# Performance work log

Measured on AMD Instinct MI355X. Metric: run time of the kernel, lower is better.

## Reference

```python
import jax, jax.numpy as jnp
import numpy as np

N, E, B, C, L, HLS = 30000, 480000, 64, 128, 3, 64
PARAM_NAMES = ['Wq','bq','Wk','bk','Wv','bv','Wskip','bskip','lstm_Wih_f','lstm_Whh_f','lstm_bih_f','lstm_bhh_f','lstm_Wih_b','lstm_Whh_b','lstm_bih_b','lstm_bhh_b','att_W','att_b','gP_W1','gP_b1','gP_W2','gP_b2','gT_W1','gT_b1','gT_W2','gT_b2','m_W0','m_b0','m_W1','m_b1','m_W2','m_b2']


def setup_inputs() -> dict:
    key = jax.random.key(0)
    ks = iter(jax.random.split(key, 64))
    rn = lambda shape: jax.random.normal(next(ks), shape, dtype=jnp.float32) * 0.05
    inp = {
        'x': jax.random.normal(next(ks), (N, C), dtype=jnp.float32),
        'edge_index': jax.random.randint(next(ks), (2, E), 0, N, dtype=jnp.int32),
        'batch': jnp.sort(jax.random.randint(next(ks), (N,), 0, B, dtype=jnp.int32)),
        'hls_attr': jax.random.normal(next(ks), (B, HLS), dtype=jnp.float32),
        'Wq': rn((L, C, C)), 'bq': rn((L, C)),
        'Wk': rn((L, C, C)), 'bk': rn((L, C)),
        'Wv': rn((L, C, C)), 'bv': rn((L, C)),
        'Wskip': rn((L, C, C)), 'bskip': rn((L, C)),
        'lstm_Wih_f': rn((4 * C, C)), 'lstm_Whh_f': rn((4 * C, C)),
        'lstm_bih_f': rn((4 * C,)), 'lstm_bhh_f': rn((4 * C,)),
        'lstm_Wih_b': rn((4 * C, C)), 'lstm_Whh_b': rn((4 * C, C)),
        'lstm_bih_b': rn((4 * C,)), 'lstm_bhh_b': rn((4 * C,)),
        'att_W': rn((2 * C, 1)), 'att_b': rn((1,)),
        'gP_W1': rn((C, C)), 'gP_b1': rn((C,)), 'gP_W2': rn((C, 1)), 'gP_b2': rn((1,)),
        'gT_W1': rn((C, C)), 'gT_b1': rn((C,)), 'gT_W2': rn((C, 1)), 'gT_b2': rn((1,)),
        'm_W0': rn((2 * C + HLS, 64)), 'm_b0': rn((64,)),
        'm_W1': rn((64, 64)), 'm_b1': rn((64,)),
        'm_W2': rn((64, 1)), 'm_b2': rn((1,)),
    }
    return inp


def _segment_softmax(logits, seg, num):
    m = jax.ops.segment_max(logits, seg, num_segments=num)
    e = jnp.exp(logits - m[seg])
    d = jax.ops.segment_sum(e, seg, num_segments=num)
    return e / d[seg]


def _lstm(xs, Wih, Whh, bih, bhh):
    # xs: [L, N, C] -> outputs [L, N, H]
    H = Whh.shape[1]
    h0 = jnp.zeros((xs.shape[1], H), xs.dtype)
    bias = bih + bhh
    def step(carry, xt):
        h, c = carry
        z = xt @ Wih.T + h @ Whh.T + bias
        i, f, g, o = jnp.split(z, 4, axis=-1)
        c = jax.nn.sigmoid(f) * c + jax.nn.sigmoid(i) * jnp.tanh(g)
        h = jax.nn.sigmoid(o) * jnp.tanh(c)
        return (h, c), h
    _, hs = jax.lax.scan(step, (h0, h0), xs)
    return hs


def _gate_pool(x, batch, W1, b1, W2, b2):
    gate = jax.nn.relu(x @ W1 + b1) @ W2 + b2          # [N, 1]
    gate = _segment_softmax(gate[:, 0], batch, B)[:, None]
    return jax.ops.segment_sum(gate * x, batch, num_segments=B)


def _forward(x, edge_index, batch, hls_attr, Wq, bq, Wk, bk, Wv, bv, Wskip, bskip,
             lstm_Wih_f, lstm_Whh_f, lstm_bih_f, lstm_bhh_f,
             lstm_Wih_b, lstm_Whh_b, lstm_bih_b, lstm_bhh_b,
             att_W, att_b, gP_W1, gP_b1, gP_W2, gP_b2, gT_W1, gT_b1, gT_W2, gT_b2,
             m_W0, m_b0, m_W1, m_b1, m_W2, m_b2):
    src, dst = edge_index[0], edge_index[1]
    scale = 1.0 / jnp.sqrt(jnp.asarray(C, jnp.float32))
    h_list = []
    for i in range(L):
        q = x @ Wq[i] + bq[i]
        k = x @ Wk[i] + bk[i]
        v = x @ Wv[i] + bv[i]
        logits = jnp.sum(q[dst] * k[src], axis=-1) * scale   # [E]
        alpha = _segment_softmax(logits, dst, N)             # per-dst softmax
        agg = jax.ops.segment_sum(alpha[:, None] * v[src], dst, num_segments=N)
        x = jax.nn.relu(agg + x @ Wskip[i] + bskip[i])       # TransformerConv + root skip, then ReLU
        h_list.append(x)
    xs = jnp.stack(h_list)                                   # [L, N, C]
    hf = _lstm(xs, lstm_Wih_f, lstm_Whh_f, lstm_bih_f, lstm_bhh_f)
    hb = _lstm(xs[::-1], lstm_Wih_b, lstm_Whh_b, lstm_bih_b, lstm_bhh_b)[::-1]
    hcat = jnp.concatenate([hf, hb], axis=-1)                # [L, N, 2C]
    a = jax.nn.softmax((hcat @ att_W)[..., 0] + att_b[0], axis=0)  # softmax over layers
    x = jnp.sum(a[..., None] * xs, axis=0)                   # [N, C] JK-LSTM output
    out_P = _gate_pool(x, batch, gP_W1, gP_b1, gP_W2, gP_b2)
    out_T = _gate_pool(x, batch, gT_W1, gT_b1, gT_W2, gT_b2)
    h = jnp.concatenate([out_P, out_T, hls_attr], axis=-1)   # [B, 2C+HLS]
    h = jax.nn.relu(h @ m_W0 + m_b0)
    h = jax.nn.relu(h @ m_W1 + m_b1)
    return h @ m_W2 + m_b2                                   # [B, 1]


def reference(x, edge_index, batch, hls_attr, Wq, bq, Wk, bk, Wv, bv, Wskip, bskip,
              lstm_Wih_f, lstm_Whh_f, lstm_bih_f, lstm_bhh_f,
              lstm_Wih_b, lstm_Whh_b, lstm_bih_b, lstm_bhh_b,
              att_W, att_b, gP_W1, gP_b1, gP_W2, gP_b2, gT_W1, gT_b1, gT_W2, gT_b2,
              m_W0, m_b0, m_W1, m_b1, m_W2, m_b2):
    return _forward(x, edge_index, batch, hls_attr, Wq, bq, Wk, bk, Wv, bv, Wskip, bskip,
                    lstm_Wih_f, lstm_Whh_f, lstm_bih_f, lstm_bhh_f,
                    lstm_Wih_b, lstm_Whh_b, lstm_bih_b, lstm_bhh_b,
                    att_W, att_b, gP_W1, gP_b1, gP_W2, gP_b2, gT_W1, gT_b1, gT_W2, gT_b2,
                    m_W0, m_b0, m_W1, m_b1, m_W2, m_b2)
```

## Files before the change

kernel.cpp:

```cpp
#include <hip/hip_runtime.h>
#include <math.h>

#define NN 30000
#define EE 480000
#define BB 64
#define CC 128
#define LLAYERS 3
#define HLSD 64
#define GXPAD 472

typedef __attribute__((ext_vector_type(8))) short bf16x8;
typedef __attribute__((ext_vector_type(4))) float f32x4;
typedef unsigned short u16;

__device__ inline unsigned short f2bf(float f){
  unsigned u = __float_as_uint(f);
  u += 0x7fffu + ((u >> 16) & 1u);
  return (unsigned short)(u >> 16);
}
__device__ inline float bf2f(unsigned short h){
  return __uint_as_float(((unsigned)h) << 16);
}
__device__ inline float fsig(float z){
  return __builtin_amdgcn_rcpf(1.f + __expf(-z));
}
__device__ inline float ftanh(float z){
  return 1.f - 2.f*__builtin_amdgcn_rcpf(1.f + __expf(2.f*z));
}

__global__ void k_hist(const int* __restrict__ dst, int* __restrict__ counts, int E){
  int e = blockIdx.x*256 + threadIdx.x;
  if (e < E) atomicAdd(&counts[dst[e]], 1);
}
__global__ void k_scan_block(const int* __restrict__ counts, int* __restrict__ row_ptr,
                             int* __restrict__ bsums, int n){
  __shared__ int sm[256];
  int i = blockIdx.x*256 + threadIdx.x;
  int v = (i < n) ? counts[i] : 0;
  sm[threadIdx.x] = v; __syncthreads();
  for (int off = 1; off < 256; off <<= 1){
    int t = (threadIdx.x >= off) ? sm[threadIdx.x - off] : 0;
    __syncthreads();
    sm[threadIdx.x] += t;
    __syncthreads();
  }
  if (i < n) row_ptr[i+1] = sm[threadIdx.x];
  if (threadIdx.x == 255) bsums[blockIdx.x] = sm[255];
}
__global__ void k_scan_bsums(const int* __restrict__ bsums, int* __restrict__ bexcl, int nb){
  int tid = threadIdx.x;
  int lane = tid & 63, wid = tid >> 6;
  int v = (tid < nb) ? bsums[tid] : 0;
  int s = v;
  #pragma unroll
  for (int o = 1; o < 64; o <<= 1){
    int t = __shfl_up(s, o, 64);
    if (lane >= o) s += t;
  }
  __shared__ int wsum[2];
  if (lane == 63) wsum[wid] = s;
  __syncthreads();
  int add = (wid == 1) ? wsum[0] : 0;
  if (tid < nb) bexcl[tid] = s - v + add;
}
__global__ void k_scan_add(int* __restrict__ row_ptr, const int* __restrict__ bexcl, int n){
  int i = blockIdx.x*256 + threadIdx.x;
  if (i < n) row_ptr[i+1] += bexcl[i >> 8];
  if (i == 0) row_ptr[0] = 0;
}
__global__ void k_fill(const int* __restrict__ src, const int* __restrict__ dst,
                       const int* __restrict__ row_ptr, int* __restrict__ fill,
                       int* __restrict__ esrc, int E){
  int e = blockIdx.x*256 + threadIdx.x;
  if (e < E){
    int d = dst[e];
    int pos = row_ptr[d] + atomicAdd(&fill[d], 1);
    esrc[pos] = src[e];
  }
}

struct PrepPtrs {
  const float* tsrc[14]; unsigned short* tdst[14];
  const float* csrc[4];  unsigned short* cdst[4];
  const float *bihf, *bhhf, *bihb, *bhhb;
  float *cbf, *cbb;
};
__global__ __launch_bounds__(256) void k_prep(PrepPtrs p){
  int b = blockIdx.x, tid = threadIdx.x;
  if (b < 14){
    const float* s = p.tsrc[b]; unsigned short* d = p.tdst[b];
    for (int i = tid; i < 16384; i += 256){
      int k = i >> 7, n = i & 127;
      d[n*128 + k] = f2bf(s[i]);
    }
  } else if (b < 30){
    int m = (b - 14) >> 2, ch = (b - 14) & 3;
    const float* s = p.csrc[m] + ch*16384; unsigned short* d = p.cdst[m] + ch*16384;
    for (int i = tid; i < 16384; i += 256) d[i] = f2bf(s[i]);
  } else {
    for (int i = tid; i < 512; i += 256){
      p.cbf[i] = p.bihf[i] + p.bhhf[i];
      p.cbb[i] = p.bihb[i] + p.bhhb[i];
    }
  }
}
__global__ __launch_bounds__(256) void k_cvt_x(const float* __restrict__ src,
                                               unsigned short* __restrict__ dst, int n8){
  int i = blockIdx.x*256 + threadIdx.x;
  if (i >= n8) return;
  float4 a = *(const float4*)(src + (size_t)i*8);
  float4 b = *(const float4*)(src + (size_t)i*8 + 4);
  union { unsigned short u[8]; uint4 v; } o;
  o.u[0]=f2bf(a.x); o.u[1]=f2bf(a.y); o.u[2]=f2bf(a.z); o.u[3]=f2bf(a.w);
  o.u[4]=f2bf(b.x); o.u[5]=f2bf(b.y); o.u[6]=f2bf(b.z); o.u[7]=f2bf(b.w);
  *(uint4*)(dst + (size_t)i*8) = o.v;
}

struct Quad { const unsigned short* Bt[4]; const float* bias[4]; };

template<int RELU, int OUTBF16>
__global__ __launch_bounds__(256) void k_mfma_gemm(
    const unsigned short* __restrict__ A0, Quad qd,
    float* __restrict__ Cf, unsigned short* __restrict__ Cb,
    int M, int ldC, int colsPerMat)
{
  __shared__ unsigned short As0[64*128];
  __shared__ unsigned short Bs0[64*128];

  const int tid = threadIdx.x;
  const int row0 = blockIdx.x*64;
  const int colg0 = blockIdx.y*64;
  const int mi = colg0 / colsPerMat;
  const int nloc = colg0 - mi*colsPerMat;
  const unsigned short* Bt0 = qd.Bt[mi];

  #pragma unroll
  for (int i = 0; i < 4; i++){
    int ch = tid + i*256;
    int r = ch >> 4, c16 = ch & 15;
    int gr = row0 + r;
    uint4 av = make_uint4(0,0,0,0);
    if (gr < M) av = *(const uint4*)(A0 + (size_t)gr*128 + c16*8);
    *(uint4*)((char*)As0 + ((r*256 + c16*16) ^ ((r&7)<<4))) = av;
    uint4 bv = *(const uint4*)(Bt0 + (size_t)(nloc + r)*128 + c16*8);
    *(uint4*)((char*)Bs0 + ((r*256 + c16*16) ^ ((r&7)<<4))) = bv;
  }
  __syncthreads();

  const int w = tid >> 6, l = tid & 63;
  const int lr = l & 15, lhi = l >> 4;

  f32x4 acc[4];
  #pragma unroll
  for (int f = 0; f < 4; f++){ acc[f][0]=0.f; acc[f][1]=0.f; acc[f][2]=0.f; acc[f][3]=0.f; }

  #pragma unroll
  for (int kt = 0; kt < 4; kt++){
    int arow = w*16 + lr;
    bf16x8 a = *(const bf16x8*)((const char*)As0 + ((arow*256 + kt*64 + lhi*16) ^ ((arow&7)<<4)));
    #pragma unroll
    for (int f = 0; f < 4; f++){
      int brow = f*16 + lr;
      bf16x8 b = *(const bf16x8*)((const char*)Bs0 + ((brow*256 + kt*64 + lhi*16) ^ ((brow&7)<<4)));
      acc[f] = __builtin_amdgcn_mfma_f32_16x16x32_bf16(a, b, acc[f], 0, 0, 0);
    }
  }

  const float* bias = qd.bias[mi];
  #pragma unroll
  for (int f = 0; f < 4; f++){
    int colg = colg0 + f*16 + lr;
    float bv = bias ? bias[nloc + f*16 + lr] : 0.f;
    #pragma unroll
    for (int r = 0; r < 4; r++){
      int grow = row0 + w*16 + lhi*4 + r;
      if (grow < M){
        float v = acc[f][r] + bv;
        if (RELU) v = fmaxf(v, 0.f);
        if (OUTBF16) Cb[(size_t)grow*ldC + colg] = f2bf(v);
        else         Cf[(size_t)grow*ldC + colg] = v;
      }
    }
  }
}

struct LstmArgs {
  const u16 *Xf, *Xb, *Hf, *Hb;
  const u16 *Wihf, *Whhf, *Wihb, *Whhb;
  const float *cbf, *cbb;
  u16 *Hof, *Hob;
  u16 *Cf, *Cb2;
  float *scF, *scB;
  const float* attW;
  int M;
};
template<int FIRST>
__global__ __launch_bounds__(256) void k_lstm2(LstmArgs a){
  __shared__ unsigned short As[64*128];
  __shared__ unsigned short Bs[128*128];
  const int bid = blockIdx.x;
  const int rowtile = bid % GXPAD;
  const int yy = bid / GXPAD;
  const int M = a.M;
  if (rowtile*64 >= M) return;
  const int dir = yy >> 2;
  const int t0 = (yy & 3)*32;
  const u16* X = dir ? a.Xb : a.Xf;
  const u16* H = dir ? a.Hb : a.Hf;
  const u16* Wih = dir ? a.Wihb : a.Wihf;
  const u16* Whh = dir ? a.Whhb : a.Whhf;
  const float* cbias = dir ? a.cbb : a.cbf;
  u16* Hout = dir ? a.Hob : a.Hof;
  u16* Cst = dir ? a.Cb2 : a.Cf;
  float* score = dir ? a.scB : a.scF;
  const float* attW = a.attW + dir*128;

  const int tid = threadIdx.x;
  const int row0 = rowtile*64;
  const int w = tid >> 6, l = tid & 63, lr = l & 15, lhi = l >> 4;

  f32x4 acc[8];
  #pragma unroll
  for (int f = 0; f < 8; f++){ acc[f][0]=0.f; acc[f][1]=0.f; acc[f][2]=0.f; acc[f][3]=0.f; }

  const int npair = FIRST ? 1 : 2;
  for (int pair = 0; pair < npair; pair++){
    const unsigned short* A  = pair ? H   : X;
    const unsigned short* Bt = pair ? Whh : Wih;
    if (pair) __syncthreads();
    #pragma unroll
    for (int i = 0; i < 4; i++){
      int ch = tid + i*256;
      int r = ch >> 4, c16 = ch & 15;
      int gr = row0 + r;
      uint4 av = make_uint4(0,0,0,0);
      if (gr < M) av = *(const uint4*)(A + (size_t)gr*128 + c16*8);
      *(uint4*)((char*)As + ((r*256 + c16*16) ^ ((r&7)<<4))) = av;
    }
    #pragma unroll
    for (int i = 0; i < 8; i++){
      int ch = tid + i*256;
      int r = ch >> 4, c16 = ch & 15;
      int gr = (r >> 5)*128 + t0 + (r & 31);
      uint4 bv = *(const uint4*)(Bt + (size_t)gr*128 + c16*8);
      *(uint4*)((char*)Bs + ((r*256 + c16*16) ^ ((r&7)<<4))) = bv;
    }
    __syncthreads();
    #pragma unroll
    for (int kt = 0; kt < 4; kt++){
      int arow = w*16 + lr;
      bf16x8 av = *(const bf16x8*)((const char*)As + ((arow*256 + kt*64 + lhi*16) ^ ((arow&7)<<4)));
      #pragma unroll
      for (int f = 0; f < 8; f++){
        int brow = f*16 + lr;
        bf16x8 bv = *(const bf16x8*)((const char*)Bs + ((brow*256 + kt*64 + lhi*16) ^ ((brow&7)<<4)));
        acc[f] = __builtin_amdgcn_mfma_f32_16x16x32_bf16(av, bv, acc[f], 0, 0, 0);
      }
    }
  }

  float sc[4] = {0.f, 0.f, 0.f, 0.f};
  #pragma unroll
  for (int cb = 0; cb < 2; cb++){
    int t = t0 + cb*16 + lr;
    float aw  = attW[t];
    float bi  = cbias[t];
    float bf_ = cbias[128 + t];
    float bg  = cbias[256 + t];
    float bo  = cbias[384 + t];
    #pragma unroll
    for (int r = 0; r < 4; r++){
      int grow = row0 + w*16 + lhi*4 + r;
      if (grow < M){
        float zi = acc[0+cb][r] + bi;
        float zf = acc[2+cb][r] + bf_;
        float zg = acc[4+cb][r] + bg;
        float zo = acc[6+cb][r] + bo;
        float cp = FIRST ? 0.f : bf2f(Cst[(size_t)grow*128 + t]);
        float cn = fsig(zf)*cp + fsig(zi)*ftanh(zg);
        float hn = fsig(zo)*ftanh(cn);
        Cst[(size_t)grow*128 + t] = f2bf(cn);
        Hout[(size_t)grow*128 + t] = f2bf(hn);
        sc[r] += hn * aw;
      }
    }
  }
  #pragma unroll
  for (int r = 0; r < 4; r++){
    float p = sc[r];
    p += __shfl_xor(p, 1, 64);
    p += __shfl_xor(p, 2, 64);
    p += __shfl_xor(p, 4, 64);
    p += __shfl_xor(p, 8, 64);
    if (lr == 0){
      int grow = row0 + w*16 + lhi*4 + r;
      if (grow < M) atomicAdd(&score[grow], p);
    }
  }
}

__global__ __launch_bounds__(256) void k_attn(
    const unsigned short* __restrict__ qkvs, const int* __restrict__ row_ptr,
    const int* __restrict__ esrc, unsigned short* __restrict__ xout, int n)
{
  int wid = threadIdx.x >> 6, lane = threadIdx.x & 63;
  int dst = blockIdx.x*4 + wid;
  if (dst >= n) return;
  const int g = lane >> 4, j = lane & 15;
  const size_t drow = (size_t)dst*512;

  bf16x8 qv = *(const bf16x8*)(qkvs + drow + j*8);
  float qf[8];
  #pragma unroll
  for (int i = 0; i < 8; i++) qf[i] = bf2f((unsigned short)qv[i]);

  const int rs = row_ptr[dst], re = row_ptr[dst+1];
  const float scale2 = 0.08838834764831845f * 1.4426950408889634f;
  float den = 0.f;
  float acc[8];
  #pragma unroll
  for (int i = 0; i < 8; i++) acc[i] = 0.f;

  int e = rs + g;
  if (e < re){
    int s = esrc[e];
    const unsigned short* sr = qkvs + (size_t)s*512 + j*8;
    bf16x8 kc = *(const bf16x8*)(sr + 128);
    bf16x8 vc = *(const bf16x8*)(sr + 256);
    while (true){
      int en = e + 4;
      bool havenext = en < re;
      bf16x8 kn, vn;
      if (havenext){
        int sn = esrc[en];
        const unsigned short* srn = qkvs + (size_t)sn*512 + j*8;
        kn = *(const bf16x8*)(srn + 128);
        vn = *(const bf16x8*)(srn + 256);
      }
      float d = qf[0]*bf2f((unsigned short)kc[0]);
      #pragma unroll
      for (int i = 1; i < 8; i++) d += qf[i]*bf2f((unsigned short)kc[i]);
      d += __shfl_xor(d, 1, 64);
      d += __shfl_xor(d, 2, 64);
      d += __shfl_xor(d, 4, 64);
      d += __shfl_xor(d, 8, 64);
      float wgt = exp2f(d * scale2);
      den += wgt;
      #pragma unroll
      for (int i = 0; i < 8; i++)
        acc[i] += wgt*bf2f((unsigned short)vc[i]);
      if (!havenext) break;
      e = en; kc = kn; vc = vn;
    }
  }

  #pragma unroll
  for (int o = 16; o <= 32; o <<= 1){
    den += __shfl_xor(den, o, 64);
    #pragma unroll
    for (int i = 0; i < 8; i++)
      acc[i] += __shfl_xor(acc[i], o, 64);
  }

  if (g == 0){
    bf16x8 sk = *(const bf16x8*)(qkvs + drow + 384 + j*8);
    float inv = (re > rs) ? 1.f/den : 0.f;
    union { unsigned short u[8]; uint4 v; } o8;
    #pragma unroll
    for (int i = 0; i < 8; i++){
      float v = acc[i]*inv + bf2f((unsigned short)sk[i]);
      o8.u[i] = f2bf(fmaxf(v, 0.f));
    }
    *(uint4*)(xout + (size_t)dst*128 + j*8) = o8.v;
  }
}

__global__ void k_jk_weights(const float* __restrict__ sF, const float* __restrict__ sB,
                             const float* __restrict__ attb, float* __restrict__ a, int n){
  int i = blockIdx.x*256 + threadIdx.x;
  if (i >= n) return;
  float s0 = sF[i]       + sB[i]       + attb[0];
  float s1 = sF[n+i]     + sB[n+i]     + attb[0];
  float s2 = sF[2*n+i]   + sB[2*n+i]   + attb[0];
  float mm = fmaxf(s0, fmaxf(s1, s2));
  float e0 = __expf(s0-mm), e1 = __expf(s1-mm), e2 = __expf(s2-mm);
  float d = e0 + e1 + e2;
  a[i] = e0/d; a[n+i] = e1/d; a[2*n+i] = e2/d;
}
__global__ void k_jk_combine(const float* __restrict__ a,
                             const unsigned short* __restrict__ x0,
                             const unsigned short* __restrict__ x1,
                             const unsigned short* __restrict__ x2,
                             float* __restrict__ xjk, unsigned short* __restrict__ xjkb, int n){
  int i8 = blockIdx.x*256 + threadIdx.x;
  if (i8 >= n*16) return;
  int node = i8 >> 4;
  float a0 = a[node], a1 = a[n+node], a2 = a[2*n+node];
  bf16x8 v0 = *(const bf16x8*)(x0 + (size_t)i8*8);
  bf16x8 v1 = *(const bf16x8*)(x1 + (size_t)i8*8);
  bf16x8 v2 = *(const bf16x8*)(x2 + (size_t)i8*8);
  float r[8];
  union { unsigned short u[8]; uint4 v; } ob;
  #pragma unroll
  for (int i = 0; i < 8; i++){
    r[i] = a0*bf2f((unsigned short)v0[i]) + a1*bf2f((unsigned short)v1[i]) + a2*bf2f((unsigned short)v2[i]);
    ob.u[i] = f2bf(r[i]);
  }
  float4* xo = (float4*)(xjk + (size_t)i8*8);
  xo[0] = make_float4(r[0], r[1], r[2], r[3]);
  xo[1] = make_float4(r[4], r[5], r[6], r[7]);
  *(uint4*)(xjkb + (size_t)i8*8) = ob.v;
}

__global__ __launch_bounds__(256) void k_rowdot2(
    const unsigned short* __restrict__ g,
    const float* __restrict__ w2P, const float* __restrict__ w2T,
    const float* __restrict__ b2P, const float* __restrict__ b2T,
    float* __restrict__ glP, float* __restrict__ glT, int n)
{
  int wid = threadIdx.x >> 6, lane = threadIdx.x & 63;
  int node = blockIdx.x*4 + wid;
  if (node >= n) return;
  ushort4 gv = *(const ushort4*)(g + (size_t)node*256 + lane*4);
  const float* w = (lane >= 32) ? w2T : w2P;
  int c0 = (lane*4) & 127;
  float4 wv = *(const float4*)(w + c0);
  float p = bf2f(gv.x)*wv.x + bf2f(gv.y)*wv.y + bf2f(gv.z)*wv.z + bf2f(gv.w)*wv.w;
  #pragma unroll
  for (int o = 1; o < 32; o <<= 1) p += __shfl_xor(p, o, 64);
  if (lane == 0)  glP[node] = p + b2P[0];
  if (lane == 32) glT[node] = p + b2T[0];
}

__global__ void k_segbounds(const int* __restrict__ batch, int* __restrict__ segp, int n){
  int i = blockIdx.x*256 + threadIdx.x;
  if (i >= n) return;
  int b = batch[i];
  int bp = (i == 0) ? -1 : batch[i-1];
  for (int s = bp+1; s <= b; s++) segp[s] = i;
  if (i == n-1){
    for (int s = b+1; s <= BB; s++) segp[s] = n;
  }
}

__global__ __launch_bounds__(256) void k_seg_stats(
    const float* __restrict__ glP, const float* __restrict__ glT,
    const int* __restrict__ segp, float4* __restrict__ stats)
{
  const int b = blockIdx.x, tid = threadIdx.x;
  const int s0 = segp[b], s1 = segp[b+1];
  __shared__ float sred[8];

  float mP = -INFINITY, mT = -INFINITY;
  for (int i = s0 + tid; i < s1; i += 256){
    mP = fmaxf(mP, glP[i]);
    mT = fmaxf(mT, glT[i]);
  }
  #pragma unroll
  for (int o = 1; o < 64; o <<= 1){
    mP = fmaxf(mP, __shfl_xor(mP, o, 64));
    mT = fmaxf(mT, __shfl_xor(mT, o, 64));
  }
  if ((tid & 63) == 0){ sred[(tid >> 6)*2] = mP; sred[(tid >> 6)*2 + 1] = mT; }
  __syncthreads();
  mP = fmaxf(fmaxf(sred[0], sred[2]), fmaxf(sred[4], sred[6]));
  mT = fmaxf(fmaxf(sred[1], sred[3]), fmaxf(sred[5], sred[7]));
  __syncthreads();

  float dP = 0.f, dT = 0.f;
  for (int i = s0 + tid; i < s1; i += 256){
    dP += __expf(glP[i] - mP);
    dT += __expf(glT[i] - mT);
  }
  #pragma unroll
  for (int o = 1; o < 64; o <<= 1){
    dP += __shfl_xor(dP, o, 64);
    dT += __shfl_xor(dT, o, 64);
  }
  if ((tid & 63) == 0){ sred[(tid >> 6)*2] = dP; sred[(tid >> 6)*2 + 1] = dT; }
  __syncthreads();
  if (tid == 0){
    dP = sred[0] + sred[2] + sred[4] + sred[6];
    dT = sred[1] + sred[3] + sred[5] + sred[7];
    float4 st;
    st.x = mP; st.y = mT;
    st.z = (dP > 0.f) ? 1.f/dP : 0.f;
    st.w = (dT > 0.f) ? 1.f/dT : 0.f;
    stats[b] = st;
  }
}

__global__ __launch_bounds__(256) void k_poolsum(
    const float* __restrict__ xjk, const int* __restrict__ segp,
    const float* __restrict__ glP, const float* __restrict__ glT,
    const float4* __restrict__ stats,
    float* __restrict__ poolP, float* __restrict__ poolT)
{
  const int b = blockIdx.x;
  const int s0 = segp[b], s1 = segp[b+1];
  const float4 st = stats[b];
  const int half = threadIdx.x >> 7, c = threadIdx.x & 127;
  const int stream = blockIdx.y*2 + half;
  float aP = 0.f, aT = 0.f;
  for (int i = s0 + stream; i < s1; i += 32){
    float eP = __expf(glP[i] - st.x);
    float eT = __expf(glT[i] - st.y);
    float xv = xjk[(size_t)i*128 + c];
    aP += eP*xv; aT += eT*xv;
  }
  if (aP != 0.f) atomicAdd(&poolP[(size_t)b*128 + c], aP*st.z);
  if (aT != 0.f) atomicAdd(&poolT[(size_t)b*128 + c], aT*st.w);
}

__global__ __launch_bounds__(64) void k_mlp(
    const float* __restrict__ poolP, const float* __restrict__ poolT, const float* __restrict__ hls,
    const float* __restrict__ W0, const float* __restrict__ b0,
    const float* __restrict__ W1, const float* __restrict__ b1,
    const float* __restrict__ W2, const float* __restrict__ b2, float* __restrict__ out)
{
  __shared__ float hin[320];
  __shared__ float h1[64];
  int b = blockIdx.x, j = threadIdx.x;
  for (int i = j; i < 320; i += 64){
    float vv;
    if (i < 128)      vv = poolP[(size_t)b*128 + i];
    else if (i < 256) vv = poolT[(size_t)b*128 + (i-128)];
    else              vv = hls[(size_t)b*64 + (i-256)];
    hin[i] = vv;
  }
  __syncthreads();
  float s = b0[j];
  for (int kk = 0; kk < 320; kk++) s += hin[kk] * W0[kk*64 + j];
  h1[j] = fmaxf(s, 0.f);
  __syncthreads();
  float s2 = b1[j];
  for (int kk = 0; kk < 64; kk++) s2 += h1[kk] * W1[kk*64 + j];
  float h2 = fmaxf(s2, 0.f);
  float p = h2 * W2[j];
  #pragma unroll
  for (int o = 1; o < 64; o <<= 1) p += __shfl_xor(p, o, 64);
  if (j == 0) out[b] = p + b2[0];
}

extern "C" void kernel_launch(void* const* d_in, const int* in_sizes, int n_in,
                              void* d_out, int out_size, void* d_ws, size_t ws_size,
                              hipStream_t stream)
{
  (void)in_sizes; (void)n_in; (void)out_size; (void)ws_size;
  const int N = NN, E = EE, C = CC;
  const float* x     = (const float*)d_in[0];
  const int*   ei    = (const int*)d_in[1];
  const int*   batch = (const int*)d_in[2];
  const float* hls   = (const float*)d_in[3];
  const float* Wq = (const float*)d_in[4],  *bq = (const float*)d_in[5];
  const float* Wk = (const float*)d_in[6],  *bk = (const float*)d_in[7];
  const float* Wv = (const float*)d_in[8],  *bv = (const float*)d_in[9];
  const float* Ws = (const float*)d_in[10], *bs = (const float*)d_in[11];
  const float* Wih_f = (const float*)d_in[12], *Whh_f = (const float*)d_in[13];
  const float* bih_f = (const float*)d_in[14], *bhh_f = (const float*)d_in[15];
  const float* Wih_b = (const float*)d_in[16], *Whh_b = (const float*)d_in[17];
  const float* bih_b = (const float*)d_in[18], *bhh_b = (const float*)d_in[19];
  const float* attW  = (const float*)d_in[20], *attb  = (const float*)d_in[21];
  const float* gPW1 = (const float*)d_in[22], *gPb1 = (const float*)d_in[23];
  const float* gPW2 = (const float*)d_in[24], *gPb2 = (const float*)d_in[25];
  const float* gTW1 = (const float*)d_in[26], *gTb1 = (const float*)d_in[27];
  const float* gTW2 = (const float*)d_in[28], *gTb2 = (const float*)d_in[29];
  const float* mW0 = (const float*)d_in[30], *mb0 = (const float*)d_in[31];
  const float* mW1 = (const float*)d_in[32], *mb1 = (const float*)d_in[33];
  const float* mW2 = (const float*)d_in[34], *mb2 = (const float*)d_in[35];
  float* out = (float*)d_out;

  const int* esrc_in = ei;
  const int* edst_in = ei + E;

  char* ws = (char*)d_ws;
  size_t off = 0;
  auto alloc = [&](size_t bytes) -> char* {
    char* p = ws + off;
    off += (bytes + 255) & ~(size_t)255;
    return p;
  };
  u16* qkvsb   = (u16*)alloc((size_t)N*512*2);
  u16* xb      = (u16*)alloc((size_t)N*C*2);
  u16* xsb0    = (u16*)alloc((size_t)N*C*2);
  u16* xsb1    = (u16*)alloc((size_t)N*C*2);
  u16* xsb2    = (u16*)alloc((size_t)N*C*2);
  u16* hfA     = (u16*)alloc((size_t)N*C*2);
  u16* hfB     = (u16*)alloc((size_t)N*C*2);
  u16* hbA     = (u16*)alloc((size_t)N*C*2);
  u16* hbB     = (u16*)alloc((size_t)N*C*2);
  u16* cfb     = (u16*)alloc((size_t)N*C*2);
  u16* cbb2    = (u16*)alloc((size_t)N*C*2);
  float* scores= (float*)alloc((size_t)6*N*4);
  float* ajk   = (float*)alloc((size_t)3*N*4);
  float* xjk   = (float*)alloc((size_t)N*C*4);
  u16* xjkb    = (u16*)alloc((size_t)N*C*2);
  u16* g1PT    = (u16*)alloc((size_t)N*256*2);
  int* counts  = (int*)alloc((size_t)N*4);
  int* row_ptr = (int*)alloc((size_t)(N+1)*4);
  int* bsums   = (int*)alloc(512);
  int* bexcl   = (int*)alloc(512);
  int* esrc    = (int*)alloc((size_t)E*4);
  float* glP   = (float*)alloc((size_t)N*4);
  float* glT   = (float*)alloc((size_t)N*4);
  int* segp    = (int*)alloc((size_t)(BB+1)*4);
  float* poolP = (float*)alloc((size_t)BB*C*4);
  float* poolT = (float*)alloc((size_t)BB*C*4);
  float4* sstats = (float4*)alloc((size_t)BB*16);
  u16* wT      = (u16*)alloc((size_t)14*16384*2);
  u16* wLSTM   = (u16*)alloc((size_t)4*65536*2);
  float* combF = (float*)alloc(512*4);
  float* combB = (float*)alloc(512*4);

  float* scF = scores;
  float* scB = scores + (size_t)3*N;

  u16* wTq = wT;
  u16* wTk = wT + 3*16384;
  u16* wTv = wT + 6*16384;
  u16* wTs = wT + 9*16384;
  u16* wTgP = wT + 12*16384;
  u16* wTgT = wT + 13*16384;
  u16* wIHf = wLSTM;
  u16* wHHf = wLSTM + 65536;
  u16* wIHb = wLSTM + 2*65536;
  u16* wHHb = wLSTM + 3*65536;

  const int NB  = (N + 255)/256;
  const int EBL = (E + 255)/256;

  PrepPtrs pp;
  for (int l = 0; l < 3; l++){
    pp.tsrc[l]   = Wq + (size_t)l*16384;  pp.tdst[l]   = wTq + (size_t)l*16384;
    pp.tsrc[3+l] = Wk + (size_t)l*16384;  pp.tdst[3+l] = wTk + (size_t)l*16384;
    pp.tsrc[6+l] = Wv + (size_t)l*16384;  pp.tdst[6+l] = wTv + (size_t)l*16384;
    pp.tsrc[9+l] = Ws + (size_t)l*16384;  pp.tdst[9+l] = wTs + (size_t)l*16384;
  }
  pp.tsrc[12] = gPW1; pp.tdst[12] = wTgP;
  pp.tsrc[13] = gTW1; pp.tdst[13] = wTgT;
  pp.csrc[0] = Wih_f; pp.cdst[0] = wIHf;
  pp.csrc[1] = Whh_f; pp.cdst[1] = wHHf;
  pp.csrc[2] = Wih_b; pp.cdst[2] = wIHb;
  pp.csrc[3] = Whh_b; pp.cdst[3] = wHHb;
  pp.bihf = bih_f; pp.bhhf = bhh_f; pp.bihb = bih_b; pp.bhhb = bhh_b;
  pp.cbf = combF; pp.cbb = combB;
  k_prep<<<31, 256, 0, stream>>>(pp);
  k_cvt_x<<<(N*C/8 + 255)/256, 256, 0, stream>>>(x, xb, N*C/8);

  hipMemsetAsync(counts, 0, (size_t)N*4, stream);
  k_hist<<<EBL, 256, 0, stream>>>(edst_in, counts, E);
  k_scan_block<<<NB, 256, 0, stream>>>(counts, row_ptr, bsums, N);
  k_scan_bsums<<<1, 128, 0, stream>>>(bsums, bexcl, NB);
  k_scan_add<<<NB, 256, 0, stream>>>(row_ptr, bexcl, N);
  hipMemsetAsync(counts, 0, (size_t)N*4, stream);
  k_fill<<<EBL, 256, 0, stream>>>(esrc_in, edst_in, row_ptr, counts, esrc, E);

  const int GX = (N + 63)/64;
  dim3 blk(256);

  u16* xsb[3] = {xsb0, xsb1, xsb2};
  const u16* ain = xb;
  for (int l = 0; l < LLAYERS; l++){
    Quad q;
    q.Bt[0] = wTq + (size_t)l*16384;  q.bias[0] = bq + (size_t)l*C;
    q.Bt[1] = wTk + (size_t)l*16384;  q.bias[1] = bk + (size_t)l*C;
    q.Bt[2] = wTv + (size_t)l*16384;  q.bias[2] = bv + (size_t)l*C;
    q.Bt[3] = wTs + (size_t)l*16384;  q.bias[3] = bs + (size_t)l*C;
    k_mfma_gemm<0,1><<<dim3(GX,8), blk, 0, stream>>>(ain, q, nullptr, qkvsb, N, 512, 128);
    k_attn<<<(N+3)/4, 256, 0, stream>>>(qkvsb, row_ptr, esrc, xsb[l], N);
    ain = xsb[l];
  }

  hipMemsetAsync(scores, 0, (size_t)6*N*4, stream);
  {
    u16* hfbuf[2] = {hfA, hfB};
    u16* hbbuf[2] = {hbA, hbB};
    for (int step = 0; step < 3; step++){
      LstmArgs la;
      la.Xf = xsb[step]; la.Xb = xsb[2-step];
      la.Hf = hfbuf[(step&1)^1]; la.Hb = hbbuf[(step&1)^1];
      la.Wihf = wIHf; la.Whhf = wHHf; la.Wihb = wIHb; la.Whhb = wHHb;
      la.cbf = combF; la.cbb = combB;
      la.Hof = hfbuf[step&1]; la.Hob = hbbuf[step&1];
      la.Cf = cfb; la.Cb2 = cbb2;
      la.scF = scF + (size_t)step*N; la.scB = scB + (size_t)(2-step)*N;
      la.attW = attW; la.M = N;
      if (step == 0) k_lstm2<1><<<dim3(GXPAD*8), blk, 0, stream>>>(la);
      else           k_lstm2<0><<<dim3(GXPAD*8), blk, 0, stream>>>(la);
    }
  }

  k_jk_weights<<<NB, 256, 0, stream>>>(scF, scB, attb, ajk, N);
  k_jk_combine<<<(N*16 + 255)/256, 256, 0, stream>>>(ajk, xsb0, xsb1, xsb2, xjk, xjkb, N);

  {
    Quad qg;
    qg.Bt[0] = wTgP; qg.bias[0] = gPb1;
    qg.Bt[1] = wTgT; qg.bias[1] = gTb1;
    qg.Bt[2] = nullptr; qg.bias[2] = nullptr;
    qg.Bt[3] = nullptr; qg.bias[3] = nullptr;
    k_mfma_gemm<1,1><<<dim3(GX,4), blk, 0, stream>>>(xjkb, qg, nullptr, g1PT, N, 256, 128);
    k_rowdot2<<<(N+3)/4, 256, 0, stream>>>(g1PT, gPW2, gTW2, gPb2, gTb2, glP, glT, N);
  }

  k_segbounds<<<NB, 256, 0, stream>>>(batch, segp, N);
  k_seg_stats<<<BB, 256, 0, stream>>>(glP, glT, segp, sstats);
  hipMemsetAsync(poolP, 0, (size_t)2*BB*C*4, stream);
  k_poolsum<<<dim3(BB,16), 256, 0, stream>>>(xjk, segp, glP, glT, sstats, poolP, poolT);

  k_mlp<<<BB, 64, 0, stream>>>(poolP, poolT, hls, mW0, mb0, mW1, mb1, mW2, mb2, out);
}
```

Baseline: 449.7 us.

## Store LSTM hidden and cell state strip-planar and prefetch recurrent operands

The LSTM h and c state buffers move from a row-major [M][128] layout to a strip-planar [4][M][32] layout. Each block now writes and reads one contiguous 32-wide plane segment instead of strided 32-column slices of 128-wide rows. The H and Whh tiles for the recurrent GEMM are loaded into registers before the input GEMM runs, so their global latency overlaps the Wih MFMA work. The cost is higher register pressure from holding 12 uint4 values per thread, and any other reader of these buffers must use the new layout.

```diff
diff --git a/kernel.cpp b/kernel.cpp
--- a/kernel.cpp
+++ b/kernel.cpp
@@ -204,7 +204,8 @@
   const int M = a.M;
   if (rowtile*64 >= M) return;
   const int dir = yy >> 2;
-  const int t0 = (yy & 3)*32;
+  const int strip = yy & 3;
+  const int t0 = strip*32;
   const u16* X = dir ? a.Xb : a.Xf;
   const u16* H = dir ? a.Hb : a.Hf;
   const u16* Wih = dir ? a.Wihb : a.Wihf;
@@ -219,31 +220,73 @@
   const int row0 = rowtile*64;
   const int w = tid >> 6, l = tid & 63, lr = l & 15, lhi = l >> 4;
 
-  f32x4 acc[8];
-  #pragma unroll
-  for (int f = 0; f < 8; f++){ acc[f][0]=0.f; acc[f][1]=0.f; acc[f][2]=0.f; acc[f][3]=0.f; }
-
-  const int npair = FIRST ? 1 : 2;
-  for (int pair = 0; pair < npair; pair++){
-    const unsigned short* A  = pair ? H   : X;
-    const unsigned short* Bt = pair ? Whh : Wih;
-    if (pair) __syncthreads();
+  #pragma unroll
+  for (int i = 0; i < 4; i++){
+    int ch = tid + i*256;
+    int r = ch >> 4, c16 = ch & 15;
+    int gr = row0 + r;
+    uint4 av = make_uint4(0,0,0,0);
+    if (gr < M) av = *(const uint4*)(X + (size_t)gr*128 + c16*8);
+    *(uint4*)((char*)As + ((r*256 + c16*16) ^ ((r&7)<<4))) = av;
+  }
+  #pragma unroll
+  for (int i = 0; i < 8; i++){
+    int ch = tid + i*256;
+    int r = ch >> 4, c16 = ch & 15;
+    int gr = (r >> 5)*128 + t0 + (r & 31);
+    uint4 bv = *(const uint4*)(Wih + (size_t)gr*128 + c16*8);
+    *(uint4*)((char*)Bs + ((r*256 + c16*16) ^ ((r&7)<<4))) = bv;
+  }
+
+  uint4 ha[4], wb[8];
+  if (!FIRST){
     #pragma unroll
     for (int i = 0; i < 4; i++){
       int ch = tid + i*256;
       int r = ch >> 4, c16 = ch & 15;
       int gr = row0 + r;
-      uint4 av = make_uint4(0,0,0,0);
-      if (gr < M) av = *(const uint4*)(A + (size_t)gr*128 + c16*8);
-      *(uint4*)((char*)As + ((r*256 + c16*16) ^ ((r&7)<<4))) = av;
+      ha[i] = make_uint4(0,0,0,0);
+      if (gr < M) ha[i] = *(const uint4*)(H + ((size_t)(c16>>2)*M + gr)*32 + (c16&3)*8);
     }
     #pragma unroll
     for (int i = 0; i < 8; i++){
       int ch = tid + i*256;
       int r = ch >> 4, c16 = ch & 15;
       int gr = (r >> 5)*128 + t0 + (r & 31);
-      uint4 bv = *(const uint4*)(Bt + (size_t)gr*128 + c16*8);
-      *(uint4*)((char*)Bs + ((r*256 + c16*16) ^ ((r&7)<<4))) = bv;
+      wb[i] = *(const uint4*)(Whh + (size_t)gr*128 + c16*8);
+    }
+  }
+  __syncthreads();
+
+  f32x4 acc[8];
+  #pragma unroll
+  for (int f = 0; f < 8; f++){ acc[f][0]=0.f; acc[f][1]=0.f; acc[f][2]=0.f; acc[f][3]=0.f; }
+
+  #pragma unroll
+  for (int kt = 0; kt < 4; kt++){
+    int arow = w*16 + lr;
+    bf16x8 av = *(const bf16x8*)((const char*)As + ((arow*256 + kt*64 + lhi*16) ^ ((arow&7)<<4)));
+    #pragma unroll
+    for (int f = 0; f < 8; f++){
+      int brow = f*16 + lr;
+      bf16x8 bv = *(const bf16x8*)((const char*)Bs + ((brow*256 + kt*64 + lhi*16) ^ ((brow&7)<<4)));
+      acc[f] = __builtin_amdgcn_mfma_f32_16x16x32_bf16(av, bv, acc[f], 0, 0, 0);
+    }
+  }
+
+  if (!FIRST){
+    __syncthreads();
+    #pragma unroll
+    for (int i = 0; i < 4; i++){
+      int ch = tid + i*256;
+      int r = ch >> 4, c16 = ch & 15;
+      *(uint4*)((char*)As + ((r*256 + c16*16) ^ ((r&7)<<4))) = ha[i];
+    }
+    #pragma unroll
+    for (int i = 0; i < 8; i++){
+      int ch = tid + i*256;
+      int r = ch >> 4, c16 = ch & 15;
+      *(uint4*)((char*)Bs + ((r*256 + c16*16) ^ ((r&7)<<4))) = wb[i];
     }
     __syncthreads();
     #pragma unroll
@@ -259,10 +302,13 @@
     }
   }
 
+  u16* Hpl = Hout + (size_t)strip*M*32;
+  u16* Cpl = Cst  + (size_t)strip*M*32;
   float sc[4] = {0.f, 0.f, 0.f, 0.f};
   #pragma unroll
   for (int cb = 0; cb < 2; cb++){
     int t = t0 + cb*16 + lr;
+    int tloc = cb*16 + lr;
     float aw  = attW[t];
     float bi  = cbias[t];
     float bf_ = cbias[128 + t];
@@ -276,11 +322,11 @@
         float zf = acc[2+cb][r] + bf_;
         float zg = acc[4+cb][r] + bg;
         float zo = acc[6+cb][r] + bo;
-        float cp = FIRST ? 0.f : bf2f(Cst[(size_t)grow*128 + t]);
+        float cp = FIRST ? 0.f : bf2f(Cpl[(size_t)grow*32 + tloc]);
         float cn = fsig(zf)*cp + fsig(zi)*ftanh(zg);
         float hn = fsig(zo)*ftanh(cn);
-        Cst[(size_t)grow*128 + t] = f2bf(cn);
-        Hout[(size_t)grow*128 + t] = f2bf(hn);
+        Cpl[(size_t)grow*32 + tloc] = f2bf(cn);
+        Hpl[(size_t)grow*32 + tloc] = f2bf(hn);
         sc[r] += hn * aw;
       }
     }
```

Result: slower. 501.5 us (+11.5%).
